# Kernel optimization log

Measured on AMD Instinct MI355X. Metric: run time of the kernel, lower is better.

## Reference

```python
import jax, jax.numpy as jnp
import numpy as np

B, S, D = 4, 2048, 1024
H, DK, DV = 16, 64, 64
LN_EPS = 1e-5


def setup_inputs() -> dict:
    key = jax.random.key(0)
    ks = jax.random.split(key, 16)
    s = 0.02
    inp = {
        "Q": jax.random.normal(ks[0], (B, S, D), jnp.float32),
        "K": jax.random.normal(ks[1], (B, S, D), jnp.float32),
        "V": jax.random.normal(ks[2], (B, S, D), jnp.float32),
        "mask": jnp.tril(jnp.ones((S, S), jnp.int32)),  # causal 2D mask
        "W_Q": jax.random.normal(ks[3], (D, H * DK), jnp.float32) * s,
        "b_Q": jnp.zeros((H * DK,), jnp.float32),
        "W_K": jax.random.normal(ks[4], (D, H * DK), jnp.float32) * s,
        "b_K": jnp.zeros((H * DK,), jnp.float32),
        "W_V": jax.random.normal(ks[5], (D, H * DV), jnp.float32) * s,
        "b_V": jnp.zeros((H * DV,), jnp.float32),
        "W_O": jax.random.normal(ks[6], (H * DV, D), jnp.float32) * s,
        "b_O": jnp.zeros((D,), jnp.float32),
        "ln_gamma": jnp.ones((D,), jnp.float32),
        "ln_beta": jnp.zeros((D,), jnp.float32),
    }
    return inp


def reference(Q, K, V, mask, W_Q, b_Q, W_K, b_K, W_V, b_V, W_O, b_O, ln_gamma, ln_beta):
    residual = Q
    # projections -> [B, H, S, d]
    q = (Q @ W_Q + b_Q).reshape(B, S, H, DK).transpose(0, 2, 1, 3)
    k = (K @ W_K + b_K).reshape(B, S, H, DK).transpose(0, 2, 1, 3)
    v = (V @ W_V + b_V).reshape(B, S, H, DV).transpose(0, 2, 1, 3)
    # scaled dot-product attention with explicit [B,H,S,S] scores
    scores = jnp.einsum("bhqd,bhkd->bhqk", q, k) / jnp.sqrt(jnp.float32(DK))
    m = mask[None, None, :, :]  # 2D mask -> [1,1,S,S] as in torch code
    scores = jnp.where(m == 0, jnp.float32(-1e9), scores)
    attn = jax.nn.softmax(scores, axis=-1)
    out = jnp.einsum("bhqk,bhkd->bhqd", attn, v)
    out = out.transpose(0, 2, 1, 3).reshape(B, S, H * DV)
    out = out @ W_O + b_O
    # layer norm over residual + out
    x = residual + out
    mu = jnp.mean(x, axis=-1, keepdims=True)
    var = jnp.mean(jnp.square(x - mu), axis=-1, keepdims=True)
    y = (x - mu) / jnp.sqrt(var + LN_EPS) * ln_gamma + ln_beta
    return y, attn
```

## Files before the change

kernel.cpp:

```cpp
#include <hip/hip_runtime.h>
#include <hip/hip_bf16.h>
#include <math.h>

#define NB 4
#define NS 2048
#define ND 1024
#define NH 16

typedef __attribute__((ext_vector_type(8))) __bf16 bf16x8;
typedef __attribute__((ext_vector_type(4))) float f32x4;
typedef __attribute__((ext_vector_type(8))) unsigned short ushort8_t;

#define VMCNT0() asm volatile("s_waitcnt vmcnt(0)" ::: "memory")
#define VMCNT2() asm volatile("s_waitcnt vmcnt(2)" ::: "memory")
#define VMCNT4() asm volatile("s_waitcnt vmcnt(4)" ::: "memory")
#define LGKM0()  asm volatile("s_waitcnt lgkmcnt(0)" ::: "memory")
#define BAR()    __builtin_amdgcn_s_barrier()

__device__ __forceinline__ unsigned short f2bf(float f){
  union { float f; unsigned int u; } v; v.f = f;
  unsigned int r = (v.u + 0x7FFFu + ((v.u >> 16) & 1u)) >> 16;
  return (unsigned short)r;
}
__device__ __forceinline__ float bf2f(unsigned short u){
  union { unsigned int i; float f; } v; v.i = ((unsigned int)u) << 16;
  return v.f;
}
__device__ __forceinline__ f32x4 mfma16(bf16x8 a, bf16x8 b, f32x4 c){
  return __builtin_amdgcn_mfma_f32_16x16x32_bf16(a, b, c, 0, 0, 0);
}
__device__ __forceinline__ bf16x8 lds_frag(const unsigned short* p){
  ushort8_t u = *reinterpret_cast<const ushort8_t*>(p);
  return __builtin_bit_cast(bf16x8, u);
}
__device__ __forceinline__ void gl16(const unsigned short* g, unsigned short* l){
  __builtin_amdgcn_global_load_lds(
      (const __attribute__((address_space(1))) void*)g,
      (__attribute__((address_space(3))) void*)l, 16, 0, 0);
}

__global__ __launch_bounds__(256)
void k_convert3(const float* __restrict__ a, const float* __restrict__ b,
                const float* __restrict__ c, unsigned short* __restrict__ oa,
                unsigned short* __restrict__ ob, unsigned short* __restrict__ oc,
                int n4){
  int i = blockIdx.x * 256 + threadIdx.x;
  if (i >= n4) return;
  const float* in = (blockIdx.y == 0) ? a : (blockIdx.y == 1) ? b : c;
  unsigned short* out = (blockIdx.y == 0) ? oa : (blockIdx.y == 1) ? ob : oc;
  float4 v = reinterpret_cast<const float4*>(in)[i];
  ushort4 o;
  o.x = f2bf(v.x); o.y = f2bf(v.y); o.z = f2bf(v.z); o.w = f2bf(v.w);
  reinterpret_cast<ushort4*>(out)[i] = o;
}

__global__ __launch_bounds__(256)
void k_transpose4(const float* __restrict__ w0, const float* __restrict__ w1,
                  const float* __restrict__ w2, const float* __restrict__ w3,
                  unsigned short* __restrict__ out){
  __shared__ float t[32][33];
  const float* in = (blockIdx.z == 0) ? w0 : (blockIdx.z == 1) ? w1 :
                    (blockIdx.z == 2) ? w2 : w3;
  unsigned short* o = out + (size_t)blockIdx.z * 1048576;
  const int k0 = blockIdx.x * 32, n0 = blockIdx.y * 32;
  const int tx = threadIdx.x & 31, ty = threadIdx.x >> 5;
  for (int r = ty; r < 32; r += 8)
    t[r][tx] = in[(size_t)(k0 + r) * 1024 + n0 + tx];
  __syncthreads();
  for (int r = ty; r < 32; r += 8)
    o[(size_t)(n0 + r) * 1024 + k0 + tx] = f2bf(t[tx][r]);
}

__global__ __launch_bounds__(256)
void k_gemm_qkv(const unsigned short* __restrict__ A0,
                const unsigned short* __restrict__ A1,
                const unsigned short* __restrict__ A2,
                const unsigned short* __restrict__ WT,
                const float* __restrict__ b0, const float* __restrict__ b1,
                const float* __restrict__ b2,
                unsigned short* __restrict__ o0,
                unsigned short* __restrict__ o1,
                unsigned short* __restrict__ o2)
{
  constexpr int K = 1024;
  __shared__ unsigned short a_s[128 * 64];
  __shared__ unsigned short b_s[128 * 64];
  const int bm = blockIdx.x;
  const int gid = blockIdx.y >> 3, bn = blockIdx.y & 7;
  const unsigned short* A = (gid == 0) ? A0 : (gid == 1) ? A1 : A2;
  const unsigned short* BT = WT + (size_t)gid * 1048576;
  const float* bias = (gid == 0) ? b0 : (gid == 1) ? b1 : b2;
  unsigned short* outp = (gid == 0) ? o0 : (gid == 1) ? o1 : o2;

  const int tid = threadIdx.x, lane = tid & 63, w = tid >> 6;
  const int wr = w >> 1, wc = w & 1;
  const int l15 = lane & 15, l4 = lane >> 4;
  const int xsw = (l15 & 7) << 3;
  const int lr = lane >> 3;
  const int scol = ((lane & 7) << 3) ^ (lr << 3);

  const f32x4 z4 = {0.f, 0.f, 0.f, 0.f};
  f32x4 acc[4][4];
  #pragma unroll
  for (int i = 0; i < 4; ++i)
    #pragma unroll
    for (int j = 0; j < 4; ++j) acc[i][j] = z4;

  const size_t abase = (size_t)(bm * 128) * K;
  const size_t bbase = (size_t)(bn * 128) * K;

  for (int kt = 0; kt < 16; ++kt){
    __syncthreads();
    #pragma unroll
    for (int i = 0; i < 4; ++i){
      const int row = w * 32 + i * 8 + lr;
      gl16(&A[abase + (size_t)row * K + kt * 64 + scol], &a_s[(w * 32 + i * 8) * 64]);
      gl16(&BT[bbase + (size_t)row * K + kt * 64 + scol], &b_s[(w * 32 + i * 8) * 64]);
    }
    __syncthreads();
    #pragma unroll
    for (int ks = 0; ks < 2; ++ks){
      const int cb = (ks * 32 + l4 * 8) ^ xsw;
      bf16x8 af[4], bfr[4];
      #pragma unroll
      for (int mf = 0; mf < 4; ++mf)
        af[mf] = lds_frag(&a_s[(wr * 64 + mf * 16 + l15) * 64 + cb]);
      #pragma unroll
      for (int nf = 0; nf < 4; ++nf)
        bfr[nf] = lds_frag(&b_s[(wc * 64 + nf * 16 + l15) * 64 + cb]);
      #pragma unroll
      for (int mf = 0; mf < 4; ++mf)
        #pragma unroll
        for (int nf = 0; nf < 4; ++nf)
          acc[mf][nf] = mfma16(af[mf], bfr[nf], acc[mf][nf]);
    }
  }

  #pragma unroll
  for (int mf = 0; mf < 4; ++mf){
    #pragma unroll
    for (int nf = 0; nf < 4; ++nf){
      const int n = bn * 128 + wc * 64 + nf * 16 + l15;
      const float bv = bias[n];
      #pragma unroll
      for (int r = 0; r < 4; ++r){
        const int m = bm * 128 + wr * 64 + mf * 16 + l4 * 4 + r;
        const float v = acc[mf][nf][r] + bv;
        const int b = m >> 11, s = m & 2047, h = n >> 6, d = n & 63;
        if (gid <= 1)
          outp[((((size_t)b * NH + h) * NS + s) << 6) + d] = f2bf(v);
        else
          outp[(((size_t)b * NH + h) * 64 + d) * NS + s] = f2bf(v);
      }
    }
  }
}

__global__ __launch_bounds__(256)
void k_gemm_o(const unsigned short* __restrict__ A,
              const unsigned short* __restrict__ BT,
              const float* __restrict__ bias,
              const float* __restrict__ resid,
              unsigned short* __restrict__ outp)
{
  constexpr int K = 1024;
  __shared__ unsigned short a_s[128 * 64];
  __shared__ unsigned short b_s[128 * 64];
  const int bm = blockIdx.x, bn = blockIdx.y;
  const int tid = threadIdx.x, lane = tid & 63, w = tid >> 6;
  const int wr = w >> 1, wc = w & 1;
  const int l15 = lane & 15, l4 = lane >> 4;
  const int xsw = (l15 & 7) << 3;
  const int lr = lane >> 3;
  const int scol = ((lane & 7) << 3) ^ (lr << 3);

  const f32x4 z4 = {0.f, 0.f, 0.f, 0.f};
  f32x4 acc[4][4];
  #pragma unroll
  for (int i = 0; i < 4; ++i)
    #pragma unroll
    for (int j = 0; j < 4; ++j) acc[i][j] = z4;

  const size_t abase = (size_t)(bm * 128) * K;
  const size_t bbase = (size_t)(bn * 128) * K;

  for (int kt = 0; kt < 16; ++kt){
    __syncthreads();
    #pragma unroll
    for (int i = 0; i < 4; ++i){
      const int row = w * 32 + i * 8 + lr;
      gl16(&A[abase + (size_t)row * K + kt * 64 + scol], &a_s[(w * 32 + i * 8) * 64]);
      gl16(&BT[bbase + (size_t)row * K + kt * 64 + scol], &b_s[(w * 32 + i * 8) * 64]);
    }
    __syncthreads();
    #pragma unroll
    for (int ks = 0; ks < 2; ++ks){
      const int cb = (ks * 32 + l4 * 8) ^ xsw;
      bf16x8 af[4], bfr[4];
      #pragma unroll
      for (int mf = 0; mf < 4; ++mf)
        af[mf] = lds_frag(&a_s[(wr * 64 + mf * 16 + l15) * 64 + cb]);
      #pragma unroll
      for (int nf = 0; nf < 4; ++nf)
        bfr[nf] = lds_frag(&b_s[(wc * 64 + nf * 16 + l15) * 64 + cb]);
      #pragma unroll
      for (int mf = 0; mf < 4; ++mf)
        #pragma unroll
        for (int nf = 0; nf < 4; ++nf)
          acc[mf][nf] = mfma16(af[mf], bfr[nf], acc[mf][nf]);
    }
  }

  #pragma unroll
  for (int mf = 0; mf < 4; ++mf){
    #pragma unroll
    for (int nf = 0; nf < 4; ++nf){
      const int n = bn * 128 + wc * 64 + nf * 16 + l15;
      const float bv = bias[n];
      #pragma unroll
      for (int r = 0; r < 4; ++r){
        const int m = bm * 128 + wr * 64 + mf * 16 + l4 * 4 + r;
        const size_t idx = (size_t)m * ND + n;
        outp[idx] = f2bf(acc[mf][nf][r] + bv + resid[idx]);
      }
    }
  }
}

__global__ __launch_bounds__(256, 4)
void k_attn(const unsigned short* __restrict__ qh,
            const unsigned short* __restrict__ kh,
            const unsigned short* __restrict__ vt,
            unsigned short* __restrict__ ctx,
            float* __restrict__ attn)
{
  __shared__ unsigned short k_s[2][64 * 64];
  __shared__ unsigned short v_s[64 * 64];
  __shared__ unsigned short p_s[64][72];

  const int id = blockIdx.x + 32 * blockIdx.y;
  const int swz = (id & 7) * 256 + (id >> 3);
  const int bh = swz >> 5;
  const int qb = 31 - (swz & 31);
  const int q0 = qb * 64;
  const int tid = threadIdx.x, lane = tid & 63, w = tid >> 6;
  const int l15 = lane & 15, l4 = lane >> 4;
  const int xsw = (l15 & 7) << 3;
  const int lr = lane >> 3;
  const int scol = ((lane & 7) << 3) ^ (lr << 3);
  const f32x4 z4 = {0.f, 0.f, 0.f, 0.f};
  const size_t kvb = (size_t)bh * NS * 64;

  bf16x8 qf[2];
  {
    const unsigned short* qp = &qh[kvb + (size_t)(q0 + w * 16 + l15) * 64];
    qf[0] = lds_frag(qp + l4 * 8);
    qf[1] = lds_frag(qp + 32 + l4 * 8);
  }

  const float SC = 0.125f * 1.44269504088896341f;
  const int ncomp = qb + 1;
  const int growb = q0 + w * 16 + l4 * 4;

  float lp[4] = {0.f, 0.f, 0.f, 0.f};

  #pragma unroll
  for (int i = 0; i < 2; ++i)
    gl16(&kh[kvb + (size_t)(w * 16 + i * 8 + lr) * 64 + scol],
         &k_s[0][(w * 16 + i * 8) * 64]);
  __syncthreads();
  int cur = 0;

  for (int kt = 0; kt < ncomp; ++kt){
    if (kt + 1 < ncomp){
      #pragma unroll
      for (int i = 0; i < 2; ++i)
        gl16(&kh[kvb + (size_t)((kt + 1) * 64 + w * 16 + i * 8 + lr) * 64 + scol],
             &k_s[cur ^ 1][(w * 16 + i * 8) * 64]);
    }
    f32x4 sc4[4];
    #pragma unroll
    for (int cf = 0; cf < 4; ++cf) sc4[cf] = z4;
    __builtin_amdgcn_s_setprio(1);
    #pragma unroll
    for (int ks = 0; ks < 2; ++ks){
      const int cb = (ks * 32 + l4 * 8) ^ xsw;
      #pragma unroll
      for (int cf = 0; cf < 4; ++cf){
        const bf16x8 bk = lds_frag(&k_s[cur][(cf * 16 + l15) * 64 + cb]);
        sc4[cf] = mfma16(qf[ks], bk, sc4[cf]);
      }
    }
    __builtin_amdgcn_s_setprio(0);
    if (kt == ncomp - 1){
      #pragma unroll
      for (int cf = 0; cf < 4; ++cf){
        const int gcol = kt * 64 + cf * 16 + l15;
        #pragma unroll
        for (int r = 0; r < 4; ++r)
          lp[r] += (gcol <= growb + r) ? exp2f(sc4[cf][r] * SC) : 0.f;
      }
    } else {
      #pragma unroll
      for (int cf = 0; cf < 4; ++cf)
        #pragma unroll
        for (int r = 0; r < 4; ++r)
          lp[r] += exp2f(sc4[cf][r] * SC);
    }
    __syncthreads();
    cur ^= 1;
  }

  float rl[4];
  #pragma unroll
  for (int r = 0; r < 4; ++r){
    float t = lp[r];
    t += __shfl_xor(t, 1);
    t += __shfl_xor(t, 2);
    t += __shfl_xor(t, 4);
    t += __shfl_xor(t, 8);
    rl[r] = 1.f / t;
  }

  f32x4 oacc[4];
  #pragma unroll
  for (int nf = 0; nf < 4; ++nf) oacc[nf] = z4;
  float* arow = attn + (size_t)bh * NS * NS;

  #pragma unroll
  for (int i = 0; i < 2; ++i)
    gl16(&kh[kvb + (size_t)(w * 16 + i * 8 + lr) * 64 + scol],
         &k_s[cur][(w * 16 + i * 8) * 64]);
  VMCNT0();
  BAR();

  for (int kt = 0; kt < ncomp; ++kt){
    const bool haveK = (kt + 1 < ncomp);
    #pragma unroll
    for (int i = 0; i < 2; ++i){
      const int row = w * 16 + i * 8 + lr;
      gl16(&vt[kvb + (size_t)row * NS + kt * 64 + scol], &v_s[(w * 16 + i * 8) * 64]);
    }
    if (haveK){
      #pragma unroll
      for (int i = 0; i < 2; ++i)
        gl16(&kh[kvb + (size_t)((kt + 1) * 64 + w * 16 + i * 8 + lr) * 64 + scol],
             &k_s[cur ^ 1][(w * 16 + i * 8) * 64]);
    }
    f32x4 sc4[4];
    #pragma unroll
    for (int cf = 0; cf < 4; ++cf) sc4[cf] = z4;
    __builtin_amdgcn_s_setprio(1);
    #pragma unroll
    for (int ks = 0; ks < 2; ++ks){
      const int cb = (ks * 32 + l4 * 8) ^ xsw;
      #pragma unroll
      for (int cf = 0; cf < 4; ++cf){
        const bf16x8 bk = lds_frag(&k_s[cur][(cf * 16 + l15) * 64 + cb]);
        sc4[cf] = mfma16(qf[ks], bk, sc4[cf]);
      }
    }
    __builtin_amdgcn_s_setprio(0);
    if (kt == ncomp - 1){
      #pragma unroll
      for (int cf = 0; cf < 4; ++cf){
        const int gcol = kt * 64 + cf * 16 + l15;
        #pragma unroll
        for (int r = 0; r < 4; ++r){
          const float a = (gcol <= growb + r) ? exp2f(sc4[cf][r] * SC) * rl[r] : 0.f;
          p_s[w * 16 + l4 * 4 + r][cf * 16 + l15] = f2bf(a);
        }
      }
    } else {
      #pragma unroll
      for (int cf = 0; cf < 4; ++cf)
        #pragma unroll
        for (int r = 0; r < 4; ++r)
          p_s[w * 16 + l4 * 4 + r][cf * 16 + l15] = f2bf(exp2f(sc4[cf][r] * SC) * rl[r]);
    }
    if (haveK){ VMCNT2(); } else { VMCNT0(); }
    LGKM0();
    BAR();
    #pragma unroll
    for (int it = 0; it < 4; ++it){
      const int row = it * 16 + (tid >> 4);
      const int c0 = (tid & 15) * 4;
      const ushort4 u = *reinterpret_cast<const ushort4*>(&p_s[row][c0]);
      float4 f4;
      f4.x = bf2f(u.x); f4.y = bf2f(u.y); f4.z = bf2f(u.z); f4.w = bf2f(u.w);
      *reinterpret_cast<float4*>(&arow[(size_t)(q0 + row) * NS + kt * 64 + c0]) = f4;
    }
    __builtin_amdgcn_s_setprio(1);
    #pragma unroll
    for (int ks2 = 0; ks2 < 2; ++ks2){
      const bf16x8 ap = lds_frag(&p_s[w * 16 + l15][ks2 * 32 + l4 * 8]);
      const int cb = (ks2 * 32 + l4 * 8) ^ xsw;
      #pragma unroll
      for (int nf = 0; nf < 4; ++nf){
        const bf16x8 bv = lds_frag(&v_s[(nf * 16 + l15) * 64 + cb]);
        oacc[nf] = mfma16(ap, bv, oacc[nf]);
      }
    }
    __builtin_amdgcn_s_setprio(0);
    if (haveK){
      VMCNT4();
      BAR();
    }
    cur ^= 1;
  }

  const int b = bh >> 4, h = bh & 15;
  #pragma unroll
  for (int nf = 0; nf < 4; ++nf){
    #pragma unroll
    for (int r = 0; r < 4; ++r){
      const int s = growb + r;
      ctx[((size_t)b * NS + s) * ND + h * 64 + nf * 16 + l15] = f2bf(oacc[nf][r]);
    }
  }

  const int zc0 = ncomp * 64;
  if (zc0 < NS){
    const float4 zz = make_float4(0.f, 0.f, 0.f, 0.f);
    for (int r = 0; r < 64; ++r){
      float* rp = arow + (size_t)(q0 + r) * NS;
      for (int c = zc0 + tid * 4; c < NS; c += 1024)
        *reinterpret_cast<float4*>(rp + c) = zz;
    }
  }
}

__global__ __launch_bounds__(256)
void k_ln(const unsigned short* __restrict__ x, const float* __restrict__ gamma,
          const float* __restrict__ beta, float* __restrict__ y){
  const int row = blockIdx.x;
  const ushort4 u = reinterpret_cast<const ushort4*>(x + (size_t)row * ND)[threadIdx.x];
  float v0 = bf2f(u.x), v1 = bf2f(u.y), v2 = bf2f(u.z), v3 = bf2f(u.w);
  float s = v0 + v1 + v2 + v3;
  float ss = v0 * v0 + v1 * v1 + v2 * v2 + v3 * v3;
  #pragma unroll
  for (int off = 32; off; off >>= 1){
    s += __shfl_xor(s, off);
    ss += __shfl_xor(ss, off);
  }
  __shared__ float rs[4], rss[4];
  const int w = threadIdx.x >> 6;
  if ((threadIdx.x & 63) == 0){ rs[w] = s; rss[w] = ss; }
  __syncthreads();
  s = rs[0] + rs[1] + rs[2] + rs[3];
  ss = rss[0] + rss[1] + rss[2] + rss[3];
  const float mu = s * (1.f / ND);
  const float var = ss * (1.f / ND) - mu * mu;
  const float rstd = rsqrtf(var + 1e-5f);
  const float4 g = reinterpret_cast<const float4*>(gamma)[threadIdx.x];
  const float4 be = reinterpret_cast<const float4*>(beta)[threadIdx.x];
  float4 o;
  o.x = (v0 - mu) * rstd * g.x + be.x;
  o.y = (v1 - mu) * rstd * g.y + be.y;
  o.z = (v2 - mu) * rstd * g.z + be.z;
  o.w = (v3 - mu) * rstd * g.w + be.w;
  reinterpret_cast<float4*>(y + (size_t)row * ND)[threadIdx.x] = o;
}

extern "C" void kernel_launch(void* const* d_in, const int* in_sizes, int n_in,
                              void* d_out, int out_size, void* d_ws, size_t ws_size,
                              hipStream_t stream){
  const float* Q   = (const float*)d_in[0];
  const float* Kin = (const float*)d_in[1];
  const float* V   = (const float*)d_in[2];
  const float* W_Q = (const float*)d_in[4];
  const float* b_Q = (const float*)d_in[5];
  const float* W_K = (const float*)d_in[6];
  const float* b_K = (const float*)d_in[7];
  const float* W_V = (const float*)d_in[8];
  const float* b_V = (const float*)d_in[9];
  const float* W_O = (const float*)d_in[10];
  const float* b_O = (const float*)d_in[11];
  const float* g   = (const float*)d_in[12];
  const float* be  = (const float*)d_in[13];

  char* ws = (char*)d_ws;
  const size_t SZ = (size_t)8192 * 1024 * 2;
  unsigned short* Qb = (unsigned short*)(ws);
  unsigned short* Kb = (unsigned short*)(ws + SZ);
  unsigned short* Vb = (unsigned short*)(ws + 2 * SZ);
  unsigned short* WT = (unsigned short*)(ws + 3 * SZ);
  unsigned short* qh = (unsigned short*)(ws + 3 * SZ + 4 * 2097152);
  unsigned short* kh = qh + (size_t)8388608;
  unsigned short* vt = kh + (size_t)8388608;
  unsigned short* ctx = Qb;
  unsigned short* x = Kb;
  float* y = (float*)d_out;
  float* attn = y + (size_t)NB * NS * ND;

  const int n4 = (NB * NS * ND) / 4;
  k_convert3<<<dim3(n4 / 256, 3), 256, 0, stream>>>(Q, Kin, V, Qb, Kb, Vb, n4);
  k_transpose4<<<dim3(32, 32, 4), 256, 0, stream>>>(W_Q, W_K, W_V, W_O, WT);

  k_gemm_qkv<<<dim3(64, 24), 256, 0, stream>>>(Qb, Kb, Vb, WT, b_Q, b_K, b_V,
                                               qh, kh, vt);

  dim3 ag(NS / 64, NB * NH);
  k_attn<<<ag, 256, 0, stream>>>(qh, kh, vt, ctx, attn);

  k_gemm_o<<<dim3(64, 8), 256, 0, stream>>>(ctx, WT + 3 * 1048576, b_O, Q, x);

  k_ln<<<NB * NS, 256, 0, stream>>>(x, g, be, y);
}
```

Before: 434.7 us.

## Double attention query tile to 128 rows per block with swizzled P buffer

```diff
diff --git a/kernel.cpp b/kernel.cpp
--- a/kernel.cpp
+++ b/kernel.cpp
@@ -13,7 +13,7 @@
 
 #define VMCNT0() asm volatile("s_waitcnt vmcnt(0)" ::: "memory")
 #define VMCNT2() asm volatile("s_waitcnt vmcnt(2)" ::: "memory")
-#define VMCNT4() asm volatile("s_waitcnt vmcnt(4)" ::: "memory")
+#define VMCNT8() asm volatile("s_waitcnt vmcnt(8)" ::: "memory")
 #define LGKM0()  asm volatile("s_waitcnt lgkmcnt(0)" ::: "memory")
 #define BAR()    __builtin_amdgcn_s_barrier()
 
@@ -236,13 +236,13 @@
 {
   __shared__ unsigned short k_s[2][64 * 64];
   __shared__ unsigned short v_s[64 * 64];
-  __shared__ unsigned short p_s[64][72];
-
-  const int id = blockIdx.x + 32 * blockIdx.y;
-  const int swz = (id & 7) * 256 + (id >> 3);
-  const int bh = swz >> 5;
-  const int qb = 31 - (swz & 31);
-  const int q0 = qb * 64;
+  __shared__ unsigned short p_s[128 * 64];
+
+  const int id = blockIdx.x + 16 * blockIdx.y;
+  const int swz = (id & 7) * 128 + (id >> 3);
+  const int bh = swz >> 4;
+  const int qb = 15 - (swz & 15);
+  const int q0 = qb * 128;
   const int tid = threadIdx.x, lane = tid & 63, w = tid >> 6;
   const int l15 = lane & 15, l4 = lane >> 4;
   const int xsw = (l15 & 7) << 3;
@@ -251,18 +251,21 @@
   const f32x4 z4 = {0.f, 0.f, 0.f, 0.f};
   const size_t kvb = (size_t)bh * NS * 64;
 
-  bf16x8 qf[2];
-  {
-    const unsigned short* qp = &qh[kvb + (size_t)(q0 + w * 16 + l15) * 64];
-    qf[0] = lds_frag(qp + l4 * 8);
-    qf[1] = lds_frag(qp + 32 + l4 * 8);
+  bf16x8 qf[2][2];
+  #pragma unroll
+  for (int mf = 0; mf < 2; ++mf){
+    const unsigned short* qp = &qh[kvb + (size_t)(q0 + w * 32 + mf * 16 + l15) * 64];
+    qf[mf][0] = lds_frag(qp + l4 * 8);
+    qf[mf][1] = lds_frag(qp + 32 + l4 * 8);
   }
 
   const float SC = 0.125f * 1.44269504088896341f;
-  const int ncomp = qb + 1;
-  const int growb = q0 + w * 16 + l4 * 4;
-
-  float lp[4] = {0.f, 0.f, 0.f, 0.f};
+  const int ncomp = 2 * qb + 2;
+  int growb[2];
+  growb[0] = q0 + w * 32 + l4 * 4;
+  growb[1] = growb[0] + 16;
+
+  float lp[2][4] = {{0.f,0.f,0.f,0.f},{0.f,0.f,0.f,0.f}};
 
   #pragma unroll
   for (int i = 0; i < 2; ++i)
@@ -278,53 +281,60 @@
         gl16(&kh[kvb + (size_t)((kt + 1) * 64 + w * 16 + i * 8 + lr) * 64 + scol],
              &k_s[cur ^ 1][(w * 16 + i * 8) * 64]);
     }
-    f32x4 sc4[4];
-    #pragma unroll
-    for (int cf = 0; cf < 4; ++cf) sc4[cf] = z4;
-    __builtin_amdgcn_s_setprio(1);
-    #pragma unroll
-    for (int ks = 0; ks < 2; ++ks){
-      const int cb = (ks * 32 + l4 * 8) ^ xsw;
-      #pragma unroll
-      for (int cf = 0; cf < 4; ++cf){
-        const bf16x8 bk = lds_frag(&k_s[cur][(cf * 16 + l15) * 64 + cb]);
-        sc4[cf] = mfma16(qf[ks], bk, sc4[cf]);
-      }
-    }
-    __builtin_amdgcn_s_setprio(0);
-    if (kt == ncomp - 1){
-      #pragma unroll
-      for (int cf = 0; cf < 4; ++cf){
-        const int gcol = kt * 64 + cf * 16 + l15;
-        #pragma unroll
-        for (int r = 0; r < 4; ++r)
-          lp[r] += (gcol <= growb + r) ? exp2f(sc4[cf][r] * SC) : 0.f;
-      }
-    } else {
-      #pragma unroll
-      for (int cf = 0; cf < 4; ++cf)
-        #pragma unroll
-        for (int r = 0; r < 4; ++r)
-          lp[r] += exp2f(sc4[cf][r] * SC);
+    #pragma unroll
+    for (int mf = 0; mf < 2; ++mf){
+      f32x4 sc4[4];
+      #pragma unroll
+      for (int cf = 0; cf < 4; ++cf) sc4[cf] = z4;
+      __builtin_amdgcn_s_setprio(1);
+      #pragma unroll
+      for (int ks = 0; ks < 2; ++ks){
+        const int cb = (ks * 32 + l4 * 8) ^ xsw;
+        #pragma unroll
+        for (int cf = 0; cf < 4; ++cf){
+          const bf16x8 bk = lds_frag(&k_s[cur][(cf * 16 + l15) * 64 + cb]);
+          sc4[cf] = mfma16(qf[mf][ks], bk, sc4[cf]);
+        }
+      }
+      __builtin_amdgcn_s_setprio(0);
+      if (kt >= ncomp - 2){
+        #pragma unroll
+        for (int cf = 0; cf < 4; ++cf){
+          const int gcol = kt * 64 + cf * 16 + l15;
+          #pragma unroll
+          for (int r = 0; r < 4; ++r)
+            lp[mf][r] += (gcol <= growb[mf] + r) ? exp2f(sc4[cf][r] * SC) : 0.f;
+        }
+      } else {
+        #pragma unroll
+        for (int cf = 0; cf < 4; ++cf)
+          #pragma unroll
+          for (int r = 0; r < 4; ++r)
+            lp[mf][r] += exp2f(sc4[cf][r] * SC);
+      }
     }
     __syncthreads();
     cur ^= 1;
   }
 
-  float rl[4];
-  #pragma unroll
-  for (int r = 0; r < 4; ++r){
-    float t = lp[r];
-    t += __shfl_xor(t, 1);
-    t += __shfl_xor(t, 2);
-    t += __shfl_xor(t, 4);
-    t += __shfl_xor(t, 8);
-    rl[r] = 1.f / t;
-  }
-
-  f32x4 oacc[4];
-  #pragma unroll
-  for (int nf = 0; nf < 4; ++nf) oacc[nf] = z4;
+  float rl[2][4];
+  #pragma unroll
+  for (int mf = 0; mf < 2; ++mf)
+    #pragma unroll
+    for (int r = 0; r < 4; ++r){
+      float t = lp[mf][r];
+      t += __shfl_xor(t, 1);
+      t += __shfl_xor(t, 2);
+      t += __shfl_xor(t, 4);
+      t += __shfl_xor(t, 8);
+      rl[mf][r] = 1.f / t;
+    }
+
+  f32x4 oacc[2][4];
+  #pragma unroll
+  for (int mf = 0; mf < 2; ++mf)
+    #pragma unroll
+    for (int nf = 0; nf < 4; ++nf) oacc[mf][nf] = z4;
   float* arow = attn + (size_t)bh * NS * NS;
 
   #pragma unroll
@@ -347,63 +357,77 @@
         gl16(&kh[kvb + (size_t)((kt + 1) * 64 + w * 16 + i * 8 + lr) * 64 + scol],
              &k_s[cur ^ 1][(w * 16 + i * 8) * 64]);
     }
-    f32x4 sc4[4];
-    #pragma unroll
-    for (int cf = 0; cf < 4; ++cf) sc4[cf] = z4;
-    __builtin_amdgcn_s_setprio(1);
-    #pragma unroll
-    for (int ks = 0; ks < 2; ++ks){
-      const int cb = (ks * 32 + l4 * 8) ^ xsw;
-      #pragma unroll
-      for (int cf = 0; cf < 4; ++cf){
-        const bf16x8 bk = lds_frag(&k_s[cur][(cf * 16 + l15) * 64 + cb]);
-        sc4[cf] = mfma16(qf[ks], bk, sc4[cf]);
-      }
-    }
-    __builtin_amdgcn_s_setprio(0);
-    if (kt == ncomp - 1){
-      #pragma unroll
-      for (int cf = 0; cf < 4; ++cf){
-        const int gcol = kt * 64 + cf * 16 + l15;
-        #pragma unroll
-        for (int r = 0; r < 4; ++r){
-          const float a = (gcol <= growb + r) ? exp2f(sc4[cf][r] * SC) * rl[r] : 0.f;
-          p_s[w * 16 + l4 * 4 + r][cf * 16 + l15] = f2bf(a);
+    #pragma unroll
+    for (int mf = 0; mf < 2; ++mf){
+      f32x4 sc4[4];
+      #pragma unroll
+      for (int cf = 0; cf < 4; ++cf) sc4[cf] = z4;
+      __builtin_amdgcn_s_setprio(1);
+      #pragma unroll
+      for (int ks = 0; ks < 2; ++ks){
+        const int cb = (ks * 32 + l4 * 8) ^ xsw;
+        #pragma unroll
+        for (int cf = 0; cf < 4; ++cf){
+          const bf16x8 bk = lds_frag(&k_s[cur][(cf * 16 + l15) * 64 + cb]);
+          sc4[cf] = mfma16(qf[mf][ks], bk, sc4[cf]);
         }
       }
-    } else {
-      #pragma unroll
-      for (int cf = 0; cf < 4; ++cf)
-        #pragma unroll
-        for (int r = 0; r < 4; ++r)
-          p_s[w * 16 + l4 * 4 + r][cf * 16 + l15] = f2bf(exp2f(sc4[cf][r] * SC) * rl[r]);
+      __builtin_amdgcn_s_setprio(0);
+      const int rbase = w * 32 + mf * 16 + l4 * 4;
+      if (kt >= ncomp - 2){
+        #pragma unroll
+        for (int cf = 0; cf < 4; ++cf){
+          const int gcol = kt * 64 + cf * 16 + l15;
+          #pragma unroll
+          for (int r = 0; r < 4; ++r){
+            const float a = (gcol <= growb[mf] + r) ? exp2f(sc4[cf][r] * SC) * rl[mf][r] : 0.f;
+            const int row = rbase + r;
+            p_s[row * 64 + ((cf * 16 + l15) ^ ((row & 7) << 3))] = f2bf(a);
+          }
+        }
+      } else {
+        #pragma unroll
+        for (int cf = 0; cf < 4; ++cf)
+          #pragma unroll
+          for (int r = 0; r < 4; ++r){
+            const float a = exp2f(sc4[cf][r] * SC) * rl[mf][r];
+            const int row = rbase + r;
+            p_s[row * 64 + ((cf * 16 + l15) ^ ((row & 7) << 3))] = f2bf(a);
+          }
+      }
     }
     if (haveK){ VMCNT2(); } else { VMCNT0(); }
     LGKM0();
     BAR();
     #pragma unroll
-    for (int it = 0; it < 4; ++it){
+    for (int it = 0; it < 8; ++it){
       const int row = it * 16 + (tid >> 4);
       const int c0 = (tid & 15) * 4;
-      const ushort4 u = *reinterpret_cast<const ushort4*>(&p_s[row][c0]);
+      const ushort4 u = *reinterpret_cast<const ushort4*>(
+          &p_s[row * 64 + (c0 ^ ((row & 7) << 3))]);
       float4 f4;
       f4.x = bf2f(u.x); f4.y = bf2f(u.y); f4.z = bf2f(u.z); f4.w = bf2f(u.w);
       *reinterpret_cast<float4*>(&arow[(size_t)(q0 + row) * NS + kt * 64 + c0]) = f4;
     }
     __builtin_amdgcn_s_setprio(1);
     #pragma unroll
-    for (int ks2 = 0; ks2 < 2; ++ks2){
-      const bf16x8 ap = lds_frag(&p_s[w * 16 + l15][ks2 * 32 + l4 * 8]);
-      const int cb = (ks2 * 32 + l4 * 8) ^ xsw;
-      #pragma unroll
-      for (int nf = 0; nf < 4; ++nf){
-        const bf16x8 bv = lds_frag(&v_s[(nf * 16 + l15) * 64 + cb]);
-        oacc[nf] = mfma16(ap, bv, oacc[nf]);
+    for (int mf = 0; mf < 2; ++mf){
+      #pragma unroll
+      for (int ks2 = 0; ks2 < 2; ++ks2){
+        const int prow = w * 32 + mf * 16 + l15;
+        const bf16x8 ap = lds_frag(
+            &p_s[prow * 64 + ((ks2 * 32 + l4 * 8) ^ ((prow & 7) << 3))]);
+        const int cb = (ks2 * 32 + l4 * 8) ^ xsw;
+        #pragma unroll
+        for (int nf = 0; nf < 4; ++nf){
+          const bf16x8 bv = lds_frag(&v_s[(nf * 16 + l15) * 64 + cb]);
+          oacc[mf][nf] = mfma16(ap, bv, oacc[mf][nf]);
+        }
       }
     }
     __builtin_amdgcn_s_setprio(0);
     if (haveK){
-      VMCNT4();
+      VMCNT8();
       BAR();
     }
     cur ^= 1;
@@ -411,18 +435,19 @@
 
   const int b = bh >> 4, h = bh & 15;
   #pragma unroll
-  for (int nf = 0; nf < 4; ++nf){
-    #pragma unroll
-    for (int r = 0; r < 4; ++r){
-      const int s = growb + r;
-      ctx[((size_t)b * NS + s) * ND + h * 64 + nf * 16 + l15] = f2bf(oacc[nf][r]);
-    }
-  }
+  for (int mf = 0; mf < 2; ++mf)
+    #pragma unroll
+    for (int nf = 0; nf < 4; ++nf)
+      #pragma unroll
+      for (int r = 0; r < 4; ++r){
+        const int s = growb[mf] + r;
+        ctx[((size_t)b * NS + s) * ND + h * 64 + nf * 16 + l15] = f2bf(oacc[mf][nf][r]);
+      }
 
   const int zc0 = ncomp * 64;
   if (zc0 < NS){
     const float4 zz = make_float4(0.f, 0.f, 0.f, 0.f);
-    for (int r = 0; r < 64; ++r){
+    for (int r = 0; r < 128; ++r){
       float* rp = arow + (size_t)(q0 + r) * NS;
       for (int c = zc0 + tid * 4; c < NS; c += 1024)
         *reinterpret_cast<float4*>(rp + c) = zz;
@@ -500,8 +525,7 @@
   k_gemm_qkv<<<dim3(64, 24), 256, 0, stream>>>(Qb, Kb, Vb, WT, b_Q, b_K, b_V,
                                                qh, kh, vt);
 
-  dim3 ag(NS / 64, NB * NH);
-  k_attn<<<ag, 256, 0, stream>>>(qh, kh, vt, ctx, attn);
+  k_attn<<<dim3(16, 64), 256, 0, stream>>>(qh, kh, vt, ctx, attn);
 
   k_gemm_o<<<dim3(64, 8), 256, 0, stream>>>(ctx, WT + 3 * 1048576, b_O, Q, x);
 
```

Result: slower. 723.6 us (+66.5%).
